# Optimization experiments

Measured on AMD Instinct MI355X. Metric: run time of the kernel, lower is better.

The kernel has to match this reference:

```python
import jax, jax.numpy as jnp
import numpy as np

N_NODES = 100000
N_EDGES = 3200000
N_GRAPHS = 1024
HID = 64
NUM_CLASSES = 21


def setup_inputs() -> dict:
    key = jax.random.key(0)
    ks = jax.random.split(key, 12)
    x = jax.random.normal(ks[0], (N_NODES, 1), dtype=jnp.float32)
    edge_index = jax.random.randint(ks[1], (2, N_EDGES), 0, N_NODES, dtype=jnp.int64)
    batch = jnp.sort(jax.random.randint(ks[2], (N_NODES,), 0, N_GRAPHS, dtype=jnp.int64))
    def lin(k, fan_in, fan_out):
        bound = 1.0 / np.sqrt(fan_in)
        return jax.random.uniform(k, (fan_in, fan_out), jnp.float32, -bound, bound)
    return {
        "x": x,
        "edge_index": edge_index,
        "batch": batch,
        # SAGEConv1: lin_l (on aggregated neighbors, with bias), lin_r (root, no bias)
        "W1l": lin(ks[3], 1, HID), "b1": jnp.zeros((HID,), jnp.float32), "W1r": lin(ks[4], 1, HID),
        # SAGEConv2
        "W2l": lin(ks[5], HID, HID), "b2": jnp.zeros((HID,), jnp.float32), "W2r": lin(ks[6], HID, HID),
        # classifier
        "Wc": lin(ks[7], HID, NUM_CLASSES), "bc": jnp.zeros((NUM_CLASSES,), jnp.float32),
    }


def _sage_conv(x, src, dst, Wl, bl, Wr):
    # mean-aggregate neighbor features: gather from src, scatter-mean to dst
    msg = x[src]                                              # [E, F] gather
    agg = jax.ops.segment_sum(msg, dst, num_segments=N_NODES)  # [N, F]
    cnt = jax.ops.segment_sum(jnp.ones((src.shape[0],), x.dtype), dst, num_segments=N_NODES)
    agg = agg / jnp.maximum(cnt, 1.0)[:, None]
    # out = lin_l(aggr) + lin_r(x)
    return agg @ Wl + bl + x @ Wr


def reference(x, edge_index, batch, W1l, b1, W1r, W2l, b2, W2r, Wc, bc):
    src, dst = edge_index[0], edge_index[1]
    h = jax.nn.relu(_sage_conv(x, src, dst, W1l, b1, W1r))
    h = jax.nn.relu(_sage_conv(h, src, dst, W2l, b2, W2r))
    # global mean pool over graphs
    pooled = jax.ops.segment_sum(h, batch, num_segments=N_GRAPHS)
    gcnt = jax.ops.segment_sum(jnp.ones((h.shape[0],), h.dtype), batch, num_segments=N_GRAPHS)
    pooled = pooled / jnp.maximum(gcnt, 1.0)[:, None]
    return pooled @ Wc + bc
```

## Files before the change

kernel.cpp:

```cpp
#include <hip/hip_runtime.h>

#define N_NODES 100000
#define N_EDGES 3200000
#define N_GRAPHS 1024
#define NCLS 21
#define NBKT 782
#define CAP 4480
#define NB 512
#define CHUNK 6250
#define TROW 72

typedef short s8v __attribute__((ext_vector_type(8)));
typedef float f4v __attribute__((ext_vector_type(4)));
typedef float f2v __attribute__((ext_vector_type(2)));

__device__ __forceinline__ float bf2f(unsigned short u) {
    return __uint_as_float(((unsigned)u) << 16);
}
__device__ __forceinline__ unsigned short f2bf(float f) {
    unsigned u = __float_as_uint(f);
    unsigned r = 0x7fffu + ((u >> 16) & 1u);
    return (unsigned short)((u + r) >> 16);
}
__device__ __forceinline__ f2v max2(f2v v) {
    f2v r; r.x = fmaxf(v.x, 0.0f); r.y = fmaxf(v.y, 0.0f); return r;
}

__global__ void k_prep(const float* __restrict__ W2l, const float* __restrict__ W2r,
                       unsigned short* __restrict__ wp,
                       const int* __restrict__ batch, int* __restrict__ gstart,
                       int* __restrict__ gcur) {
    if (blockIdx.x < 32) {
        int tid = blockIdx.x * 256 + threadIdx.x;
        int frag = tid >> 9;
        int r = tid & 511;
        int L = r >> 3, j = r & 7;
        int kstep = frag >> 2, nt = frag & 3;
        int k = kstep * 32 + (L >> 4) * 8 + j;
        int n = nt * 16 + (L & 15);
        float val = (k < 64) ? W2l[k * 64 + n] : W2r[(k - 64) * 64 + n];
        wp[tid] = f2bf(val);
    } else if (blockIdx.x < 37) {
        int g = (blockIdx.x - 32) * 256 + threadIdx.x;
        if (g > N_GRAPHS) return;
        if (g == N_GRAPHS) { gstart[N_GRAPHS] = N_NODES; return; }
        int lo = 0, hi = N_NODES;
        while (lo < hi) { int m = (lo + hi) >> 1; if (batch[m] < g) lo = m + 1; else hi = m; }
        gstart[g] = lo;
    } else {
        for (int i = threadIdx.x; i < NBKT; i += 256) gcur[i] = i * CAP;
    }
}

__global__ __launch_bounds__(256) void k_binone(const int* __restrict__ src,
                                                const int* __restrict__ dst,
                                                int* __restrict__ gcur,
                                                unsigned int* __restrict__ bins) {
    __shared__ unsigned int ebuf[CHUNK];
    __shared__ unsigned short bbuf[CHUNK];
    __shared__ int lh[NBKT];
    __shared__ int lbase[NBKT];
    int t = threadIdx.x;
    for (int i = t; i < NBKT; i += 256) lh[i] = 0;
    __syncthreads();
    const int2* s2 = (const int2*)(src + blockIdx.x * CHUNK);
    const int2* d2 = (const int2*)(dst + blockIdx.x * CHUNK);
    for (int i = t; i < CHUNK / 2; i += 256) {
        int2 s = s2[i];
        int2 d = d2[i];
        uint2 pp;
        pp.x = ((unsigned)s.x << 7) | (unsigned)(d.x & 127);
        pp.y = ((unsigned)s.y << 7) | (unsigned)(d.y & 127);
        *(uint2*)(&ebuf[2 * i]) = pp;
        bbuf[2 * i]     = (unsigned short)(d.x >> 7);
        bbuf[2 * i + 1] = (unsigned short)(d.y >> 7);
        atomicAdd(&lh[d.x >> 7], 1);
        atomicAdd(&lh[d.y >> 7], 1);
    }
    __syncthreads();
    for (int i = t; i < NBKT; i += 256)
        lbase[i] = atomicAdd(&gcur[i], lh[i]);
    __syncthreads();
    for (int i = t; i < NBKT; i += 256) lh[i] = lbase[i];
    __syncthreads();
    for (int i = t; i < CHUNK; i += 256) {
        int b = (int)bbuf[i];
        int pos = atomicAdd(&lh[b], 1);
        if (pos < (b + 1) * CAP) bins[pos] = ebuf[i];
    }
}

__global__ __launch_bounds__(256) void k_build(
    const int* __restrict__ gcur, unsigned int* __restrict__ bins,
    int* __restrict__ row, unsigned short* __restrict__ deg,
    const float* __restrict__ x, float2* __restrict__ ax) {
    __shared__ unsigned int ebuf[CAP];
    __shared__ int hist[128];
    __shared__ int curs[128];
    __shared__ int lds[128];
    __shared__ float t1[128];
    int k = blockIdx.x, t = threadIdx.x;
    int e0 = k * CAP;
    int cnt = min(gcur[k] - e0, CAP);
    if (t < 128) { hist[t] = 0; t1[t] = 0.0f; }
    __syncthreads();
    for (int i = t; i < cnt; i += 256) {
        unsigned p = bins[e0 + i];
        ebuf[i] = p;
        atomicAdd(&hist[p & 127u], 1);
    }
    __syncthreads();
    if (t < 128) lds[t] = hist[t];
    __syncthreads();
    for (int off = 1; off < 128; off <<= 1) {
        int cur = (t < 128) ? lds[t] : 0;
        int add = (t < 128 && t >= off) ? lds[t - off] : 0;
        __syncthreads();
        if (t < 128) lds[t] = cur + add;
        __syncthreads();
    }
    if (t < 128) {
        int run = e0 + lds[t] - hist[t];
        curs[t] = run;
        int n = k * 128 + t;
        if (n < N_NODES) { row[n] = run; deg[n] = (unsigned short)hist[t]; }
    }
    __syncthreads();
    for (int i = t; i < cnt; i += 256) {
        unsigned p = ebuf[i];
        int slot = (int)(p & 127u);
        int pos = atomicAdd(&curs[slot], 1);
        bins[pos] = p >> 7;
        atomicAdd(&t1[slot], x[p >> 7]);
    }
    __syncthreads();
    if (t < 128) {
        int n = k * 128 + t;
        if (n < N_NODES) {
            float a = t1[t] / fmaxf((float)hist[t], 1.0f);
            float2 v; v.x = a; v.y = x[n];
            ax[n] = v;
        }
    }
}

__global__ __launch_bounds__(256) void k_l2f(
    const int* __restrict__ row, const unsigned short* __restrict__ deg,
    const unsigned int* __restrict__ csr,
    const float2* __restrict__ ax,
    const float* __restrict__ W1l, const float* __restrict__ b1,
    const float* __restrict__ W1r,
    const unsigned short* __restrict__ wp, const float* __restrict__ b2,
    unsigned short* __restrict__ h2b) {
    __shared__ unsigned short tile[4][16 * TROW];
    int wid = threadIdx.x >> 6;
    int w = blockIdx.x * 4 + wid;
    if (w >= N_NODES / 16) return;
    int L = threadIdx.x & 63;
    int fo = L & 7;
    int g  = L >> 3;
    unsigned short* tw = tile[wid];

    f2v w1l_[4], w1r_[4], bb_[4];
    {
        const f2v* pl = (const f2v*)(W1l + fo * 8);
        const f2v* pr = (const f2v*)(W1r + fo * 8);
        const f2v* pb = (const f2v*)(b1  + fo * 8);
#pragma unroll
        for (int q = 0; q < 4; q++) { w1l_[q] = pl[q]; w1r_[q] = pr[q]; bb_[q] = pb[q]; }
    }

    int nA = w * 16 + g;
    int nB = nA + 8;
    int r0A = row[nA]; int dnA = (int)deg[nA];
    int r0B = row[nB]; int dnB = (int)deg[nB];

#define SWZ(v, j) __builtin_amdgcn_ds_swizzle((v), (((j) << 5) | 0x18))
#define EDGE(j) { \
    unsigned au = (unsigned)SWZ((int)__float_as_uint(pr0.x), j); \
    unsigned xu = (unsigned)SWZ((int)__float_as_uint(pr0.y), j); \
    float a_ = __uint_as_float(au), x_ = __uint_as_float(xu); \
    f2v av; av.x = a_; av.y = a_; \
    f2v xv; xv.x = x_; xv.y = x_; \
    pp0 += max2(av * w1l_[0] + (xv * w1r_[0] + bb_[0])); \
    pp1 += max2(av * w1l_[1] + (xv * w1r_[1] + bb_[1])); \
    pp2 += max2(av * w1l_[2] + (xv * w1r_[2] + bb_[2])); \
    pp3 += max2(av * w1l_[3] + (xv * w1r_[3] + bb_[3])); }
#define REM(j) if ((j) < rem) EDGE(j)

#pragma unroll
    for (int pass = 0; pass < 2; pass++) {
        int r0 = pass ? r0B : r0A;
        int dn = pass ? dnB : dnA;
        int trow = g + 8 * pass;
        int r1 = r0 + dn;
        f2v pp0 = {0.f, 0.f}, pp1 = pp0, pp2 = pp0, pp3 = pp0;
        int base = r0;
        int c0 = max(min(base + fo, r1 - 1), r0);
        unsigned i0 = min((unsigned)csr[c0], (unsigned)(N_NODES - 1));
        float2 pr0 = ax[i0];
        int c1 = max(min(base + 8 + fo, r1 - 1), r0);
        unsigned i1 = min((unsigned)csr[c1], (unsigned)(N_NODES - 1));
        while (base + 8 <= r1) {
            float2 prn = ax[i1];
            int c2 = max(min(base + 16 + fo, r1 - 1), r0);
            unsigned i2 = min((unsigned)csr[c2], (unsigned)(N_NODES - 1));
            EDGE(0) EDGE(1) EDGE(2) EDGE(3)
            EDGE(4) EDGE(5) EDGE(6) EDGE(7)
            pr0 = prn; i1 = i2; base += 8;
        }
        int rem = r1 - base;
        if (rem > 0) {
            REM(0) REM(1) REM(2) REM(3)
            REM(4) REM(5) REM(6) REM(7)
        }
        float inv = 1.0f / fmaxf((float)dn, 1.0f);
        f2v iv; iv.x = inv; iv.y = inv;
        pp0 *= iv; pp1 *= iv; pp2 *= iv; pp3 *= iv;
        unsigned w0 = (unsigned)f2bf(pp0.x) | ((unsigned)f2bf(pp0.y) << 16);
        unsigned w1 = (unsigned)f2bf(pp1.x) | ((unsigned)f2bf(pp1.y) << 16);
        unsigned w2 = (unsigned)f2bf(pp2.x) | ((unsigned)f2bf(pp2.y) << 16);
        unsigned w3 = (unsigned)f2bf(pp3.x) | ((unsigned)f2bf(pp3.y) << 16);
        uint4 pk; pk.x = w0; pk.y = w1; pk.z = w2; pk.w = w3;
        *(uint4*)(tw + trow * TROW + fo * 8) = pk;
    }
#undef SWZ
#undef EDGE
#undef REM

    int m = L & 15, q = L >> 4;
    int nrow = w * 16 + m;

    const s8v a0 = *(const s8v*)(tw + m * TROW + q * 8);
    const s8v a1 = *(const s8v*)(tw + m * TROW + 32 + q * 8);

    float2 axn = ax[nrow];
    union { s8v v; unsigned u[4]; } A2, A3;
    {
        const f2v* l1 = (const f2v*)(W1l + q * 8);
        const f2v* r1p = (const f2v*)(W1r + q * 8);
        const f2v* bp = (const f2v*)(b1 + q * 8);
        const f2v* l2 = (const f2v*)(W1l + 32 + q * 8);
        const f2v* r2p = (const f2v*)(W1r + 32 + q * 8);
        const f2v* b2p = (const f2v*)(b1 + 32 + q * 8);
        f2v av; av.x = axn.x; av.y = axn.x;
        f2v xv; xv.x = axn.y; xv.y = axn.y;
#pragma unroll
        for (int k = 0; k < 4; k++) {
            f2v v1 = max2(av * l1[k] + (xv * r1p[k] + bp[k]));
            f2v v2 = max2(av * l2[k] + (xv * r2p[k] + b2p[k]));
            A2.u[k] = (unsigned)f2bf(v1.x) | ((unsigned)f2bf(v1.y) << 16);
            A3.u[k] = (unsigned)f2bf(v2.x) | ((unsigned)f2bf(v2.y) << 16);
        }
    }
    const s8v a2 = A2.v;
    const s8v a3 = A3.v;

#define LOADB(i) s8v B##i = *(const s8v*)(wp + (i) * 512 + L * 8)
    LOADB(0); LOADB(1); LOADB(2); LOADB(3);
    LOADB(4); LOADB(5); LOADB(6); LOADB(7);
    LOADB(8); LOADB(9); LOADB(10); LOADB(11);
    LOADB(12); LOADB(13); LOADB(14); LOADB(15);
#undef LOADB

    f4v acc0 = {0.f, 0.f, 0.f, 0.f}, acc1 = acc0, acc2 = acc0, acc3 = acc0;
    acc0 = __builtin_amdgcn_mfma_f32_16x16x32_bf16(a0, B0,  acc0, 0, 0, 0);
    acc0 = __builtin_amdgcn_mfma_f32_16x16x32_bf16(a1, B4,  acc0, 0, 0, 0);
    acc0 = __builtin_amdgcn_mfma_f32_16x16x32_bf16(a2, B8,  acc0, 0, 0, 0);
    acc0 = __builtin_amdgcn_mfma_f32_16x16x32_bf16(a3, B12, acc0, 0, 0, 0);
    acc1 = __builtin_amdgcn_mfma_f32_16x16x32_bf16(a0, B1,  acc1, 0, 0, 0);
    acc1 = __builtin_amdgcn_mfma_f32_16x16x32_bf16(a1, B5,  acc1, 0, 0, 0);
    acc1 = __builtin_amdgcn_mfma_f32_16x16x32_bf16(a2, B9,  acc1, 0, 0, 0);
    acc1 = __builtin_amdgcn_mfma_f32_16x16x32_bf16(a3, B13, acc1, 0, 0, 0);
    acc2 = __builtin_amdgcn_mfma_f32_16x16x32_bf16(a0, B2,  acc2, 0, 0, 0);
    acc2 = __builtin_amdgcn_mfma_f32_16x16x32_bf16(a1, B6,  acc2, 0, 0, 0);
    acc2 = __builtin_amdgcn_mfma_f32_16x16x32_bf16(a2, B10, acc2, 0, 0, 0);
    acc2 = __builtin_amdgcn_mfma_f32_16x16x32_bf16(a3, B14, acc2, 0, 0, 0);
    acc3 = __builtin_amdgcn_mfma_f32_16x16x32_bf16(a0, B3,  acc3, 0, 0, 0);
    acc3 = __builtin_amdgcn_mfma_f32_16x16x32_bf16(a1, B7,  acc3, 0, 0, 0);
    acc3 = __builtin_amdgcn_mfma_f32_16x16x32_bf16(a2, B11, acc3, 0, 0, 0);
    acc3 = __builtin_amdgcn_mfma_f32_16x16x32_bf16(a3, B15, acc3, 0, 0, 0);

    int fcol = L & 15;
    float bia0 = b2[fcol], bia1 = b2[16 + fcol], bia2 = b2[32 + fcol], bia3 = b2[48 + fcol];
    int rbase = w * 16 + q * 4;
#pragma unroll
    for (int r = 0; r < 4; r++) {
        size_t o = (size_t)(rbase + r) * 64 + fcol;
        h2b[o]      = f2bf(fmaxf(acc0[r] + bia0, 0.0f));
        h2b[o + 16] = f2bf(fmaxf(acc1[r] + bia1, 0.0f));
        h2b[o + 32] = f2bf(fmaxf(acc2[r] + bia2, 0.0f));
        h2b[o + 48] = f2bf(fmaxf(acc3[r] + bia3, 0.0f));
    }
}

__global__ __launch_bounds__(256) void k_head(
    const unsigned short* __restrict__ h2b, const int* __restrict__ gstart,
    const float* __restrict__ Wc, const float* __restrict__ bc,
    float* __restrict__ out) {
    __shared__ float part[4][64];
    __shared__ float rowv[64];
    int g = blockIdx.x;
    int wid = threadIdx.x >> 6;
    int f = threadIdx.x & 63;
    int ns = gstart[g], ne = gstart[g + 1];
    float s = 0.0f;
    int n = ns + wid;
    for (; n + 12 < ne; n += 16) {
        float v0 = bf2f(h2b[(size_t)(n)      * 64 + f]);
        float v1 = bf2f(h2b[(size_t)(n + 4)  * 64 + f]);
        float v2 = bf2f(h2b[(size_t)(n + 8)  * 64 + f]);
        float v3 = bf2f(h2b[(size_t)(n + 12) * 64 + f]);
        s += (v0 + v1) + (v2 + v3);
    }
    for (; n < ne; n += 4) s += bf2f(h2b[(size_t)n * 64 + f]);
    part[wid][f] = s;
    __syncthreads();
    if (threadIdx.x < 64) {
        float tot = part[0][f] + part[1][f] + part[2][f] + part[3][f];
        rowv[f] = tot / fmaxf((float)(ne - ns), 1.0f);
    }
    __syncthreads();
    if (threadIdx.x < NCLS) {
        float acc = bc[threadIdx.x];
#pragma unroll
        for (int kk = 0; kk < 64; kk++) acc += rowv[kk] * Wc[kk * NCLS + threadIdx.x];
        out[g * NCLS + threadIdx.x] = acc;
    }
}

extern "C" void kernel_launch(void* const* d_in, const int* in_sizes, int n_in,
                              void* d_out, int out_size, void* d_ws, size_t ws_size,
                              hipStream_t stream) {
    const float* x     = (const float*)d_in[0];
    const int*   eidx  = (const int*)d_in[1];
    const int*   batch = (const int*)d_in[2];
    const float* W1l   = (const float*)d_in[3];
    const float* b1    = (const float*)d_in[4];
    const float* W1r   = (const float*)d_in[5];
    const float* W2l   = (const float*)d_in[6];
    const float* b2    = (const float*)d_in[7];
    const float* W2r   = (const float*)d_in[8];
    const float* Wc    = (const float*)d_in[9];
    const float* bc    = (const float*)d_in[10];
    float* out = (float*)d_out;

    const int* src = eidx;
    const int* dst = eidx + N_EDGES;

    char* p = (char*)d_ws;
    unsigned int* bins  = (unsigned int*)p;     p += (size_t)NBKT * CAP * 4;
    float2* ax          = (float2*)p;           p += (size_t)N_NODES * 8;
    unsigned short* h2b = (unsigned short*)p;   p += (size_t)N_NODES * 64 * 2;
    int* row   = (int*)p;                       p += (size_t)(N_NODES + 1) * 4;
    unsigned short* deg = (unsigned short*)p;   p += (size_t)N_NODES * 2;
    int* gcur  = (int*)p;                       p += NBKT * 4;
    int* gstart= (int*)p;                       p += (N_GRAPHS + 1) * 4;
    unsigned short* wp = (unsigned short*)p;    p += 8192 * 2;

    k_prep  <<<38, 256, 0, stream>>>(W2l, W2r, wp, batch, gstart, gcur);
    k_binone<<<NB, 256, 0, stream>>>(src, dst, gcur, bins);
    k_build <<<NBKT, 256, 0, stream>>>(gcur, bins, row, deg, x, ax);
    k_l2f   <<<(N_NODES / 16 + 3) / 4, 256, 0, stream>>>(row, deg, bins, ax,
                                                          W1l, b1, W1r, wp, b2, h2b);
    k_head  <<<N_GRAPHS, 256, 0, stream>>>(h2b, gstart, Wc, bc, out);
}
```

Baseline: 208.4 us.

## Build CSR with global-atomic counting sort instead of bucketed LDS binning

Replaces the two-stage bucket binning and per-bucket LDS sort with a degree count plus first-layer sum using global atomics, a wave-scan row allocation, and a global-atomic scatter into CSR. This simplifies the pipeline and removes the fixed bucket capacity. In exchange it adds millions of contended global atomics and random writes. Row order is now set by atomic allocation, and edge order within a row is nondeterministic.

```diff
diff --git a/kernel.cpp b/kernel.cpp
--- a/kernel.cpp
+++ b/kernel.cpp
@@ -4,10 +4,6 @@
 #define N_EDGES 3200000
 #define N_GRAPHS 1024
 #define NCLS 21
-#define NBKT 782
-#define CAP 4480
-#define NB 512
-#define CHUNK 6250
 #define TROW 72
 
 typedef short s8v __attribute__((ext_vector_type(8)));
@@ -29,7 +25,8 @@
 __global__ void k_prep(const float* __restrict__ W2l, const float* __restrict__ W2r,
                        unsigned short* __restrict__ wp,
                        const int* __restrict__ batch, int* __restrict__ gstart,
-                       int* __restrict__ gcur) {
+                       int* __restrict__ deg32, float* __restrict__ aggs,
+                       int* __restrict__ total) {
     if (blockIdx.x < 32) {
         int tid = blockIdx.x * 256 + threadIdx.x;
         int frag = tid >> 9;
@@ -48,100 +45,75 @@
         while (lo < hi) { int m = (lo + hi) >> 1; if (batch[m] < g) lo = m + 1; else hi = m; }
         gstart[g] = lo;
     } else {
-        for (int i = threadIdx.x; i < NBKT; i += 256) gcur[i] = i * CAP;
-    }
-}
-
-__global__ __launch_bounds__(256) void k_binone(const int* __restrict__ src,
-                                                const int* __restrict__ dst,
-                                                int* __restrict__ gcur,
-                                                unsigned int* __restrict__ bins) {
-    __shared__ unsigned int ebuf[CHUNK];
-    __shared__ unsigned short bbuf[CHUNK];
-    __shared__ int lh[NBKT];
-    __shared__ int lbase[NBKT];
-    int t = threadIdx.x;
-    for (int i = t; i < NBKT; i += 256) lh[i] = 0;
-    __syncthreads();
-    const int2* s2 = (const int2*)(src + blockIdx.x * CHUNK);
-    const int2* d2 = (const int2*)(dst + blockIdx.x * CHUNK);
-    for (int i = t; i < CHUNK / 2; i += 256) {
-        int2 s = s2[i];
-        int2 d = d2[i];
-        uint2 pp;
-        pp.x = ((unsigned)s.x << 7) | (unsigned)(d.x & 127);
-        pp.y = ((unsigned)s.y << 7) | (unsigned)(d.y & 127);
-        *(uint2*)(&ebuf[2 * i]) = pp;
-        bbuf[2 * i]     = (unsigned short)(d.x >> 7);
-        bbuf[2 * i + 1] = (unsigned short)(d.y >> 7);
-        atomicAdd(&lh[d.x >> 7], 1);
-        atomicAdd(&lh[d.y >> 7], 1);
-    }
-    __syncthreads();
-    for (int i = t; i < NBKT; i += 256)
-        lbase[i] = atomicAdd(&gcur[i], lh[i]);
-    __syncthreads();
-    for (int i = t; i < NBKT; i += 256) lh[i] = lbase[i];
-    __syncthreads();
-    for (int i = t; i < CHUNK; i += 256) {
-        int b = (int)bbuf[i];
-        int pos = atomicAdd(&lh[b], 1);
-        if (pos < (b + 1) * CAP) bins[pos] = ebuf[i];
-    }
-}
-
-__global__ __launch_bounds__(256) void k_build(
-    const int* __restrict__ gcur, unsigned int* __restrict__ bins,
-    int* __restrict__ row, unsigned short* __restrict__ deg,
-    const float* __restrict__ x, float2* __restrict__ ax) {
-    __shared__ unsigned int ebuf[CAP];
-    __shared__ int hist[128];
-    __shared__ int curs[128];
-    __shared__ int lds[128];
-    __shared__ float t1[128];
-    int k = blockIdx.x, t = threadIdx.x;
-    int e0 = k * CAP;
-    int cnt = min(gcur[k] - e0, CAP);
-    if (t < 128) { hist[t] = 0; t1[t] = 0.0f; }
-    __syncthreads();
-    for (int i = t; i < cnt; i += 256) {
-        unsigned p = bins[e0 + i];
-        ebuf[i] = p;
-        atomicAdd(&hist[p & 127u], 1);
-    }
-    __syncthreads();
-    if (t < 128) lds[t] = hist[t];
-    __syncthreads();
-    for (int off = 1; off < 128; off <<= 1) {
-        int cur = (t < 128) ? lds[t] : 0;
-        int add = (t < 128 && t >= off) ? lds[t - off] : 0;
-        __syncthreads();
-        if (t < 128) lds[t] = cur + add;
-        __syncthreads();
-    }
-    if (t < 128) {
-        int run = e0 + lds[t] - hist[t];
-        curs[t] = run;
-        int n = k * 128 + t;
-        if (n < N_NODES) { row[n] = run; deg[n] = (unsigned short)hist[t]; }
-    }
-    __syncthreads();
-    for (int i = t; i < cnt; i += 256) {
-        unsigned p = ebuf[i];
-        int slot = (int)(p & 127u);
-        int pos = atomicAdd(&curs[slot], 1);
-        bins[pos] = p >> 7;
-        atomicAdd(&t1[slot], x[p >> 7]);
-    }
-    __syncthreads();
-    if (t < 128) {
-        int n = k * 128 + t;
-        if (n < N_NODES) {
-            float a = t1[t] / fmaxf((float)hist[t], 1.0f);
-            float2 v; v.x = a; v.y = x[n];
-            ax[n] = v;
-        }
-    }
+        int n = (blockIdx.x - 37) * 256 + threadIdx.x;
+        if (n < N_NODES) { deg32[n] = 0; aggs[n] = 0.0f; }
+        if (blockIdx.x == 37 && threadIdx.x == 0) total[0] = 0;
+    }
+}
+
+__global__ __launch_bounds__(256) void k_count(const int* __restrict__ src,
+                                               const int* __restrict__ dst,
+                                               const float* __restrict__ x,
+                                               int* __restrict__ deg32,
+                                               float* __restrict__ aggs) {
+    int i = blockIdx.x * 256 + threadIdx.x;
+    int4 d = ((const int4*)dst)[i];
+    int4 s = ((const int4*)src)[i];
+    float x0 = x[s.x], x1 = x[s.y], x2 = x[s.z], x3 = x[s.w];
+    atomicAdd(&deg32[d.x], 1);
+    atomicAdd(&deg32[d.y], 1);
+    atomicAdd(&deg32[d.z], 1);
+    atomicAdd(&deg32[d.w], 1);
+    atomicAdd(&aggs[d.x], x0);
+    atomicAdd(&aggs[d.y], x1);
+    atomicAdd(&aggs[d.z], x2);
+    atomicAdd(&aggs[d.w], x3);
+}
+
+__global__ __launch_bounds__(256) void k_alloc(const int* __restrict__ deg32,
+                                               const float* __restrict__ aggs,
+                                               const float* __restrict__ x,
+                                               int* __restrict__ row, int* __restrict__ cur,
+                                               unsigned short* __restrict__ deg,
+                                               float2* __restrict__ ax,
+                                               int* __restrict__ total) {
+    int n = blockIdx.x * 256 + threadIdx.x;
+    int lane = threadIdx.x & 63;
+    int d = (n < N_NODES) ? deg32[n] : 0;
+    int pre = d;
+#pragma unroll
+    for (int off = 1; off < 64; off <<= 1) {
+        int v = __shfl_up(pre, off, 64);
+        if (lane >= off) pre += v;
+    }
+    int wavetot = __shfl(pre, 63, 64);
+    int base = 0;
+    if (lane == 63) base = atomicAdd(total, wavetot);
+    base = __shfl(base, 63, 64);
+    if (n < N_NODES) {
+        int r = base + pre - d;
+        row[n] = r; cur[n] = r;
+        deg[n] = (unsigned short)d;
+        float2 v; v.x = aggs[n] / fmaxf((float)d, 1.0f); v.y = x[n];
+        ax[n] = v;
+    }
+}
+
+__global__ __launch_bounds__(256) void k_scatter(const int* __restrict__ src,
+                                                 const int* __restrict__ dst,
+                                                 int* __restrict__ cur,
+                                                 int* __restrict__ csr) {
+    int i = blockIdx.x * 256 + threadIdx.x;
+    int4 d = ((const int4*)dst)[i];
+    int4 s = ((const int4*)src)[i];
+    int p0 = atomicAdd(&cur[d.x], 1);
+    int p1 = atomicAdd(&cur[d.y], 1);
+    int p2 = atomicAdd(&cur[d.z], 1);
+    int p3 = atomicAdd(&cur[d.w], 1);
+    csr[p0] = s.x;
+    csr[p1] = s.y;
+    csr[p2] = s.z;
+    csr[p3] = s.w;
 }
 
 __global__ __launch_bounds__(256) void k_l2f(
@@ -349,19 +321,25 @@
     const int* dst = eidx + N_EDGES;
 
     char* p = (char*)d_ws;
-    unsigned int* bins  = (unsigned int*)p;     p += (size_t)NBKT * CAP * 4;
+    int* csr            = (int*)p;              p += (size_t)(N_EDGES + 64) * 4;
     float2* ax          = (float2*)p;           p += (size_t)N_NODES * 8;
     unsigned short* h2b = (unsigned short*)p;   p += (size_t)N_NODES * 64 * 2;
-    int* row   = (int*)p;                       p += (size_t)(N_NODES + 1) * 4;
+    int* row   = (int*)p;                       p += (size_t)N_NODES * 4;
     unsigned short* deg = (unsigned short*)p;   p += (size_t)N_NODES * 2;
-    int* gcur  = (int*)p;                       p += NBKT * 4;
+    int* deg32 = (int*)p;                       p += (size_t)N_NODES * 4;
+    float* aggs= (float*)p;                     p += (size_t)N_NODES * 4;
+    int* cur   = (int*)p;                       p += (size_t)N_NODES * 4;
+    int* total = (int*)p;                       p += 256;
     int* gstart= (int*)p;                       p += (N_GRAPHS + 1) * 4;
     unsigned short* wp = (unsigned short*)p;    p += 8192 * 2;
 
-    k_prep  <<<38, 256, 0, stream>>>(W2l, W2r, wp, batch, gstart, gcur);
-    k_binone<<<NB, 256, 0, stream>>>(src, dst, gcur, bins);
-    k_build <<<NBKT, 256, 0, stream>>>(gcur, bins, row, deg, x, ax);
-    k_l2f   <<<(N_NODES / 16 + 3) / 4, 256, 0, stream>>>(row, deg, bins, ax,
-                                                          W1l, b1, W1r, wp, b2, h2b);
-    k_head  <<<N_GRAPHS, 256, 0, stream>>>(h2b, gstart, Wc, bc, out);
-}
+    k_prep   <<<37 + (N_NODES + 255) / 256, 256, 0, stream>>>(W2l, W2r, wp, batch,
+                                                              gstart, deg32, aggs, total);
+    k_count  <<<N_EDGES / 1024, 256, 0, stream>>>(src, dst, x, deg32, aggs);
+    k_alloc  <<<(N_NODES + 255) / 256, 256, 0, stream>>>(deg32, aggs, x, row, cur,
+                                                         deg, ax, total);
+    k_scatter<<<N_EDGES / 1024, 256, 0, stream>>>(src, dst, cur, csr);
+    k_l2f    <<<(N_NODES / 16 + 3) / 4, 256, 0, stream>>>(row, deg, (const unsigned int*)csr,
+                                                          ax, W1l, b1, W1r, wp, b2, h2b);
+    k_head   <<<N_GRAPHS, 256, 0, stream>>>(h2b, gstart, Wc, bc, out);
+}
```

After: 713.1 us. +242.2%, slower.
